# Optimization experiments

Hardware: AMD Instinct MI355X
Metric: run time of the kernel (lower is better)

The kernel has to match this reference:

```python
import jax, jax.numpy as jnp
import numpy as np

N = 100000


def gcn_conv(x, edge_index, W, b):
    """PyG GCNConv: h = D^-1/2 (A+I) D^-1/2 (x W) + b, scatter-add at targets."""
    n = x.shape[0]
    src, dst = edge_index[0], edge_index[1]
    # add self-loops
    loop = jnp.arange(n, dtype=src.dtype)
    src = jnp.concatenate([src, loop])
    dst = jnp.concatenate([dst, loop])
    # degree of target nodes (with self-loops), symmetric normalization
    deg = jax.ops.segment_sum(jnp.ones_like(dst, dtype=x.dtype), dst, num_segments=n)
    dinv = jnp.where(deg > 0, jax.lax.rsqrt(deg), 0.0)
    norm = dinv[src] * dinv[dst]                     # [E+N]
    h = x @ W                                        # [N, out] transform first (small dim)
    msg = h[src] * norm[:, None]                     # gather + scale
    out = jax.ops.segment_sum(msg, dst, num_segments=n)  # scatter-add
    return out + b


def setup_inputs() -> dict:
    key = jax.random.key(0)
    k1, k2, k3, k4, k5 = jax.random.split(key, 5)
    x = jax.random.normal(k1, (N, 128), dtype=jnp.float32)
    edge_index = jax.random.randint(k2, (2, 1600000), 0, N, dtype=jnp.int64)
    # glorot-ish init for linear weights, zero bias (PyG default)
    W1 = jax.random.normal(k3, (128, 64), dtype=jnp.float32) * (1.0 / np.sqrt(128))
    b1 = jnp.zeros((64,), dtype=jnp.float32)
    W2 = jax.random.normal(k4, (64, 32), dtype=jnp.float32) * (1.0 / np.sqrt(64))
    b2 = jnp.zeros((32,), dtype=jnp.float32)
    return {"x": x, "edge_index": edge_index, "W1": W1, "b1": b1, "W2": W2, "b2": b2}


def reference(x, edge_index, W1, b1, W2, b2):
    h = gcn_conv(x, edge_index, W1, b1)
    h = jax.nn.relu(h)
    # dropout is identity in eval mode (training=False)
    out = gcn_conv(h, edge_index, W2, b2)
    return out
```

## Files before the change

kernel.cpp:

```cpp
#include <hip/hip_runtime.h>

typedef unsigned int   u32;
typedef unsigned short u16;
typedef __attribute__((ext_vector_type(8))) short bf16x8;
typedef __attribute__((ext_vector_type(4))) float f32x4;

__device__ __forceinline__ u16 f2b(float f) {
    u32 u = __float_as_uint(f);
    u += 0x7FFFu + ((u >> 16) & 1u);
    return (u16)(u >> 16);
}
__device__ __forceinline__ float b2f_lo(u32 v) { return __uint_as_float(v << 16); }
__device__ __forceinline__ float b2f_hi(u32 v) { return __uint_as_float(v & 0xFFFF0000u); }
__device__ __forceinline__ u32 pack2(float a, float b) {
    return (u32)f2b(a) | ((u32)f2b(b) << 16);
}

#define BSHIFT 8
#define BIN_CHUNK 2048
#define CAP_MAX 6144


__global__ void k_init(const float* __restrict__ W1, bf16x8* __restrict__ Wpack,
                       int* __restrict__ bcnt, int NB) {
    int tid = threadIdx.x;
    for (int i = tid; i < NB; i += 256) bcnt[i] = 0;
    if (tid < 64) {
        int lane = tid;
#pragma unroll
        for (int ct = 0; ct < 4; ct++) {
#pragma unroll
            for (int ks = 0; ks < 4; ks++) {
                bf16x8 h;
#pragma unroll
                for (int j = 0; j < 8; j++) {
                    int k = ks * 32 + ((lane >> 4) << 3) + j;
                    int col = ct * 16 + (lane & 15);
                    h[j] = (short)f2b(W1[k * 64 + col]);
                }
                Wpack[(ct * 4 + ks) * 64 + lane] = h;
            }
        }
    }
}


__global__ __launch_bounds__(256) void k_bin(const int* __restrict__ src,
                                             const int* __restrict__ dst,
                                             int* __restrict__ bcnt,
                                             u32* __restrict__ binned,
                                             int E, int NB, int CAP) {
    __shared__ int lh[512], ls[512], gb[512], sh[256];
    __shared__ u32 stage[BIN_CHUNK];
    __shared__ u16 sbuck[BIN_CHUNK];
    int tid = threadIdx.x;
    int base = blockIdx.x * BIN_CHUNK;
    int cnt = E - base;
    if (cnt > BIN_CHUNK) cnt = BIN_CHUNK;

    for (int i = tid; i < 512; i += 256) lh[i] = 0;
    __syncthreads();

    const int T = BIN_CHUNK / 256;
    int bk[T], r[T];
    u32 key[T];
#pragma unroll
    for (int t = 0; t < T; t++) {
        int i = base + t * 256 + tid;
        bk[t] = -1;
        if (i < E) {
            int dv = dst[i];
            bk[t] = dv >> BSHIFT;
            key[t] = ((u32)(dv & 255) << 24) | (u32)src[i];
            r[t] = atomicAdd(&lh[bk[t]], 1);
        }
    }
    __syncthreads();
    {
        int a0 = lh[2 * tid], a1 = lh[2 * tid + 1];
        int sum2 = a0 + a1;
        sh[tid] = sum2;
        __syncthreads();
        for (int dd = 1; dd < 256; dd <<= 1) {
            int x = tid >= dd ? sh[tid - dd] : 0;
            __syncthreads();
            sh[tid] += x;
            __syncthreads();
        }
        int excl = sh[tid] - sum2;
        ls[2 * tid] = excl;
        ls[2 * tid + 1] = excl + a0;
    }
    for (int b = tid; b < NB; b += 256) {
        int c = lh[b];
        gb[b] = c ? atomicAdd(&bcnt[b], c) : 0;
    }
    __syncthreads();
#pragma unroll
    for (int t = 0; t < T; t++) {
        if (bk[t] >= 0) {
            int slot = ls[bk[t]] + r[t];
            stage[slot] = key[t];
            sbuck[slot] = (u16)bk[t];
        }
    }
    __syncthreads();
    for (int j = tid; j < cnt; j += 256) {
        u32 e = stage[j];
        int b = sbuck[j];
        int p = gb[b] + (j - ls[b]);
        if (p < CAP) binned[(size_t)b * CAP + p] = e;
    }
}


__global__ __launch_bounds__(256) void k_csr_gemm1(const u32* __restrict__ binned,
                                                   const int* __restrict__ bcnt,
                                                   const bf16x8* __restrict__ Wpack,
                                                   const float* __restrict__ x,
                                                   float* __restrict__ dinv,
                                                   int2* __restrict__ offse,
                                                   int* __restrict__ esrc,
                                                   u16* __restrict__ h1b,
                                                   int n, int CAP) {
    __shared__ u32 stagec[CAP_MAX];
    __shared__ int lcnt[256], lcur[256], sh[256];
    __shared__ float dinv_sh[256];
    int tid = threadIdx.x;
    int b = blockIdx.x;
    size_t base = (size_t)b * CAP;
    int nodeBase = b << BSHIFT;
    int ecnt = bcnt[b];
    if (ecnt > CAP) ecnt = CAP;
    lcnt[tid] = 0;
    __syncthreads();
    for (int j = tid; j < ecnt; j += 256) {
        u32 e = binned[base + j];
        stagec[j] = e;
        atomicAdd(&lcnt[e >> 24], 1);
    }
    __syncthreads();
    int v = lcnt[tid];
    sh[tid] = v;
    __syncthreads();
    for (int d = 1; d < 256; d <<= 1) {
        int xx = tid >= d ? sh[tid - d] : 0;
        __syncthreads();
        sh[tid] += xx;
        __syncthreads();
    }
    int excl = sh[tid] - v;
    int node = nodeBase + tid;
    float dvt = rsqrtf((float)(v + 1));
    dinv_sh[tid] = dvt;
    if (node < n) {
        offse[node] = make_int2((int)base + excl, (int)base + excl + v);
        dinv[node] = dvt;
    }
    lcur[tid] = excl;
    __syncthreads();
    for (int j = tid; j < ecnt; j += 256) {
        u32 e = stagec[j];
        int p = atomicAdd(&lcur[e >> 24], 1);
        esrc[base + p] = (int)(e & 0xFFFFFFu);
    }

    int wv = tid >> 6, lane = tid & 63;
    bf16x8 bfr[16];
#pragma unroll
    for (int f = 0; f < 16; f++) bfr[f] = Wpack[f * 64 + lane];

    for (int t = wv; t < 16; t += 4) {
        int rowBase = nodeBase + t * 16;
        if (rowBase >= n) break;
        f32x4 acc[4];
#pragma unroll
        for (int ct = 0; ct < 4; ct++) acc[ct] = (f32x4){0.f, 0.f, 0.f, 0.f};

        int r0 = rowBase + (lane & 15);
        if (r0 >= n) r0 = n - 1;
        const float* xr = x + (size_t)r0 * 128 + ((lane >> 4) << 3);
#pragma unroll
        for (int ks = 0; ks < 4; ks++) {
            float4 p0 = *(const float4*)(xr + ks * 32);
            float4 p1 = *(const float4*)(xr + ks * 32 + 4);
            bf16x8 a;
            a[0] = (short)f2b(p0.x); a[1] = (short)f2b(p0.y);
            a[2] = (short)f2b(p0.z); a[3] = (short)f2b(p0.w);
            a[4] = (short)f2b(p1.x); a[5] = (short)f2b(p1.y);
            a[6] = (short)f2b(p1.z); a[7] = (short)f2b(p1.w);
#pragma unroll
            for (int ct = 0; ct < 4; ct++)
                acc[ct] = __builtin_amdgcn_mfma_f32_16x16x32_bf16(a, bfr[ct * 4 + ks], acc[ct], 0, 0, 0);
        }
        int lrb = t * 16 + ((lane >> 4) << 2);
#pragma unroll
        for (int r = 0; r < 4; r++) {
            int lrow = lrb + r;
            int row = nodeBase + lrow;
            float dv = dinv_sh[lrow];
#pragma unroll
            for (int ct = 0; ct < 4; ct++) {
                float o = acc[ct][r] * dv;
                float onb = __shfl_xor(o, 1);
                if (!(lane & 1) && row < n) {
                    *(u32*)&h1b[(size_t)row * 64 + ct * 16 + (lane & 15)] = pack2(o, onb);
                }
            }
        }
    }
}


__global__ __launch_bounds__(256) void k_agg1gemm2(const u16* __restrict__ h1b,
                                                   const int2* __restrict__ offse,
                                                   const int* __restrict__ esrc,
                                                   const float* __restrict__ dinv,
                                                   const float* __restrict__ b1,
                                                   const float* __restrict__ W2,
                                                   u16* __restrict__ h2b, int n) {
    __shared__ float aggL[4][64];
    int warp = threadIdx.x >> 6, lane = threadIdx.x & 63;
    int half = lane >> 5, c2 = lane & 31;
    float w2r[32];
#pragma unroll
    for (int kk = 0; kk < 32; kk++) w2r[kk] = W2[(half * 32 + kk) * 32 + c2];
    float2 bb = *(const float2*)&b1[2 * c2];
    int nwaves = (gridDim.x * blockDim.x) >> 6;
    for (int wid = (int)((blockIdx.x * blockDim.x + threadIdx.x) >> 6); wid < n;
         wid += nwaves) {
        int2 ov = offse[wid];
        int e1 = ov.y;
        float a0 = 0.f, a1 = 0.f, a2 = 0.f, a3 = 0.f;
        if (half == 0) {
            u32 v = *(const u32*)&h1b[(size_t)wid * 64 + 2 * c2];
            a0 += b2f_lo(v); a1 += b2f_hi(v);
        }
        int e = ov.x + half;
        for (; e + 2 < e1; e += 4) {
            int s0 = esrc[e], s1 = esrc[e + 2];
            u32 v0 = *(const u32*)&h1b[(size_t)s0 * 64 + 2 * c2];
            u32 v1 = *(const u32*)&h1b[(size_t)s1 * 64 + 2 * c2];
            a0 += b2f_lo(v0); a1 += b2f_hi(v0);
            a2 += b2f_lo(v1); a3 += b2f_hi(v1);
        }
        if (e < e1) {
            int s = esrc[e];
            u32 v = *(const u32*)&h1b[(size_t)s * 64 + 2 * c2];
            a0 += b2f_lo(v); a1 += b2f_hi(v);
        }
        a0 += a2; a1 += a3;
        a0 += __shfl_xor(a0, 32);
        a1 += __shfl_xor(a1, 32);
        float dv = dinv[wid];
        a0 = a0 * dv + bb.x; a1 = a1 * dv + bb.y;
        a0 = a0 > 0.f ? a0 : 0.f;
        a1 = a1 > 0.f ? a1 : 0.f;
        if (half == 0) *(float2*)&aggL[warp][2 * c2] = make_float2(a0, a1);
        asm volatile("s_waitcnt lgkmcnt(0)" ::: "memory");
        float acc = 0.f;
#pragma unroll
        for (int kk = 0; kk < 32; kk += 4) {
            float4 av = *(const float4*)&aggL[warp][half * 32 + kk];
            acc += av.x * w2r[kk] + av.y * w2r[kk + 1] + av.z * w2r[kk + 2] + av.w * w2r[kk + 3];
        }
        acc += __shfl_xor(acc, 32);
        if (half == 0) h2b[(size_t)wid * 32 + c2] = f2b(acc * dv);
    }
}


__global__ __launch_bounds__(256) void k_agg2(const u16* __restrict__ h2b,
                                              const int2* __restrict__ offse,
                                              const int* __restrict__ esrc,
                                              const float* __restrict__ dinv,
                                              const float* __restrict__ b2,
                                              float* __restrict__ out, int n) {
    int wid = (int)((blockIdx.x * blockDim.x + threadIdx.x) >> 6);
    int lane = threadIdx.x & 63;
    int g = lane >> 4, c2 = lane & 15;
    if (wid >= n) return;
    int2 ov = offse[wid];
    int e1 = ov.y;
    float a0 = 0.f, a1 = 0.f, a2 = 0.f, a3 = 0.f;
    int e = ov.x + g;
    for (; e + 4 < e1; e += 8) {
        int s0 = esrc[e], s1 = esrc[e + 4];
        u32 v0 = *(const u32*)&h2b[(size_t)s0 * 32 + 2 * c2];
        u32 v1 = *(const u32*)&h2b[(size_t)s1 * 32 + 2 * c2];
        a0 += b2f_lo(v0); a1 += b2f_hi(v0);
        a2 += b2f_lo(v1); a3 += b2f_hi(v1);
    }
    if (e < e1) {
        int s = esrc[e];
        u32 v = *(const u32*)&h2b[(size_t)s * 32 + 2 * c2];
        a0 += b2f_lo(v); a1 += b2f_hi(v);
    }
    a0 += a2; a1 += a3;
    a0 += __shfl_xor(a0, 16); a0 += __shfl_xor(a0, 32);
    a1 += __shfl_xor(a1, 16); a1 += __shfl_xor(a1, 32);
    if (g == 0) {
        u32 v = *(const u32*)&h2b[(size_t)wid * 32 + 2 * c2];
        a0 += b2f_lo(v); a1 += b2f_hi(v);
        float dv = dinv[wid];
        float2 o = make_float2(a0 * dv + b2[2 * c2], a1 * dv + b2[2 * c2 + 1]);
        *(float2*)&out[(size_t)wid * 32 + 2 * c2] = o;
    }
}


extern "C" void kernel_launch(void* const* d_in, const int* in_sizes, int n_in,
                              void* d_out, int out_size, void* d_ws, size_t ws_size,
                              hipStream_t stream) {
    const float* x  = (const float*)d_in[0];
    const int*   ei = (const int*)d_in[1];
    const float* W1 = (const float*)d_in[2];
    const float* b1 = (const float*)d_in[3];
    const float* W2 = (const float*)d_in[4];
    const float* b2 = (const float*)d_in[5];
    float* out = (float*)d_out;

    const int n = in_sizes[0] / 128;
    const int E = in_sizes[1] / 2;
    const int* src = ei;
    const int* dst = ei + E;
    const int NB = (n + 255) >> BSHIFT;
    int avg = (E + NB - 1) / NB;
    int CAP = avg + avg / 8 + 512;
    if (CAP > CAP_MAX) CAP = CAP_MAX;

    char* ws = (char*)d_ws;
    size_t woff = 0;
    auto carve = [&](size_t bytes) {
        void* p = ws + woff;
        woff += (bytes + 255) & ~(size_t)255;
        return p;
    };
    int*    bcnt   = (int*)carve((size_t)NB * sizeof(int));
    u32*    binned = (u32*)carve((size_t)NB * CAP * sizeof(u32));
    int2*   offse  = (int2*)carve((size_t)n * sizeof(int2));
    float*  dinv   = (float*)carve((size_t)n * sizeof(float));
    int*    esrc   = (int*)carve((size_t)NB * CAP * sizeof(int));
    bf16x8* Wpack  = (bf16x8*)carve(16 * 64 * sizeof(bf16x8));
    u16*    h1b    = (u16*)carve((size_t)n * 64 * sizeof(u16));
    u16*    h2b    = (u16*)carve((size_t)n * 32 * sizeof(u16));

    const int B = 256;

    k_init<<<1, B, 0, stream>>>(W1, Wpack, bcnt, NB);

    k_bin<<<(E + BIN_CHUNK - 1) / BIN_CHUNK, B, 0, stream>>>(src, dst, bcnt, binned, E, NB, CAP);

    k_csr_gemm1<<<NB, B, 0, stream>>>(binned, bcnt, Wpack, x, dinv, offse, esrc, h1b, n, CAP);

    k_agg1gemm2<<<2048, B, 0, stream>>>(h1b, offse, esrc, dinv, b1, W2, h2b, n);

    k_agg2<<<(n + 3) / 4, B, 0, stream>>>(h2b, offse, esrc, dinv, b2, out, n);
}
```

Measured before the change: 164.7 us.

## Split layer-1 aggregation into column-chunked gathers and an MFMA GEMM2

```diff
diff --git a/kernel.cpp b/kernel.cpp
--- a/kernel.cpp
+++ b/kernel.cpp
@@ -21,7 +21,8 @@
 #define CAP_MAX 6144
 
 
-__global__ void k_init(const float* __restrict__ W1, bf16x8* __restrict__ Wpack,
+__global__ void k_init(const float* __restrict__ W1, const float* __restrict__ W2,
+                       bf16x8* __restrict__ Wpack, bf16x8* __restrict__ W2pack,
                        int* __restrict__ bcnt, int NB) {
     int tid = threadIdx.x;
     for (int i = tid; i < NB; i += 256) bcnt[i] = 0;
@@ -39,6 +40,20 @@
                     h[j] = (short)f2b(W1[k * 64 + col]);
                 }
                 Wpack[(ct * 4 + ks) * 64 + lane] = h;
+            }
+        }
+#pragma unroll
+        for (int ct = 0; ct < 2; ct++) {
+#pragma unroll
+            for (int ks = 0; ks < 2; ks++) {
+                bf16x8 h;
+#pragma unroll
+                for (int j = 0; j < 8; j++) {
+                    int k = ks * 32 + ((lane >> 4) << 3) + j;
+                    int col = ct * 16 + (lane & 15);
+                    h[j] = (short)f2b(W2[k * 32 + col]);
+                }
+                W2pack[(ct * 2 + ks) * 64 + lane] = h;
             }
         }
     }
@@ -169,6 +184,7 @@
     bf16x8 bfr[16];
 #pragma unroll
     for (int f = 0; f < 16; f++) bfr[f] = Wpack[f * 64 + lane];
+    size_t cs = (size_t)n * 16;
 
     for (int t = wv; t < 16; t += 4) {
         int rowBase = nodeBase + t * 16;
@@ -204,7 +220,7 @@
                 float o = acc[ct][r] * dv;
                 float onb = __shfl_xor(o, 1);
                 if (!(lane & 1) && row < n) {
-                    *(u32*)&h1b[(size_t)row * 64 + ct * 16 + (lane & 15)] = pack2(o, onb);
+                    *(u32*)&h1b[(size_t)ct * cs + (size_t)row * 16 + (lane & 15)] = pack2(o, onb);
                 }
             }
         }
@@ -212,60 +228,94 @@
 }
 
 
-__global__ __launch_bounds__(256) void k_agg1gemm2(const u16* __restrict__ h1b,
-                                                   const int2* __restrict__ offse,
-                                                   const int* __restrict__ esrc,
-                                                   const float* __restrict__ dinv,
-                                                   const float* __restrict__ b1,
-                                                   const float* __restrict__ W2,
-                                                   u16* __restrict__ h2b, int n) {
-    __shared__ float aggL[4][64];
-    int warp = threadIdx.x >> 6, lane = threadIdx.x & 63;
-    int half = lane >> 5, c2 = lane & 31;
-    float w2r[32];
-#pragma unroll
-    for (int kk = 0; kk < 32; kk++) w2r[kk] = W2[(half * 32 + kk) * 32 + c2];
-    float2 bb = *(const float2*)&b1[2 * c2];
-    int nwaves = (gridDim.x * blockDim.x) >> 6;
-    for (int wid = (int)((blockIdx.x * blockDim.x + threadIdx.x) >> 6); wid < n;
-         wid += nwaves) {
-        int2 ov = offse[wid];
-        int e1 = ov.y;
-        float a0 = 0.f, a1 = 0.f, a2 = 0.f, a3 = 0.f;
-        if (half == 0) {
-            u32 v = *(const u32*)&h1b[(size_t)wid * 64 + 2 * c2];
-            a0 += b2f_lo(v); a1 += b2f_hi(v);
-        }
-        int e = ov.x + half;
-        for (; e + 2 < e1; e += 4) {
-            int s0 = esrc[e], s1 = esrc[e + 2];
-            u32 v0 = *(const u32*)&h1b[(size_t)s0 * 64 + 2 * c2];
-            u32 v1 = *(const u32*)&h1b[(size_t)s1 * 64 + 2 * c2];
-            a0 += b2f_lo(v0); a1 += b2f_hi(v0);
-            a2 += b2f_lo(v1); a3 += b2f_hi(v1);
-        }
-        if (e < e1) {
-            int s = esrc[e];
-            u32 v = *(const u32*)&h1b[(size_t)s * 64 + 2 * c2];
-            a0 += b2f_lo(v); a1 += b2f_hi(v);
-        }
-        a0 += a2; a1 += a3;
-        a0 += __shfl_xor(a0, 32);
-        a1 += __shfl_xor(a1, 32);
-        float dv = dinv[wid];
-        a0 = a0 * dv + bb.x; a1 = a1 * dv + bb.y;
-        a0 = a0 > 0.f ? a0 : 0.f;
-        a1 = a1 > 0.f ? a1 : 0.f;
-        if (half == 0) *(float2*)&aggL[warp][2 * c2] = make_float2(a0, a1);
-        asm volatile("s_waitcnt lgkmcnt(0)" ::: "memory");
-        float acc = 0.f;
-#pragma unroll
-        for (int kk = 0; kk < 32; kk += 4) {
-            float4 av = *(const float4*)&aggL[warp][half * 32 + kk];
-            acc += av.x * w2r[kk] + av.y * w2r[kk + 1] + av.z * w2r[kk + 2] + av.w * w2r[kk + 3];
-        }
-        acc += __shfl_xor(acc, 32);
-        if (half == 0) h2b[(size_t)wid * 32 + c2] = f2b(acc * dv);
+__global__ __launch_bounds__(256) void k_gather1(const u16* __restrict__ h1c,
+                                                 const int2* __restrict__ offse,
+                                                 const int* __restrict__ esrc,
+                                                 float* __restrict__ aggc,
+                                                 int n) {
+    int node = (int)((blockIdx.x * blockDim.x + threadIdx.x) >> 5);
+    if (node >= n) return;
+    int l = threadIdx.x & 31;
+    int slot = l >> 3;
+    int j = l & 7;
+    int2 ov = offse[node];
+    float a0 = 0.f, a1 = 0.f;
+    for (int e = ov.x + slot; e < ov.y; e += 4) {
+        int s = esrc[e];
+        u32 v = *(const u32*)&h1c[(size_t)s * 16 + 2 * j];
+        a0 += b2f_lo(v); a1 += b2f_hi(v);
+    }
+    a0 += __shfl_xor(a0, 8);  a1 += __shfl_xor(a1, 8);
+    a0 += __shfl_xor(a0, 16); a1 += __shfl_xor(a1, 16);
+    if (slot == 0) {
+        u32 v = *(const u32*)&h1c[(size_t)node * 16 + 2 * j];
+        a0 += b2f_lo(v); a1 += b2f_hi(v);
+        *(float2*)&aggc[(size_t)node * 16 + 2 * j] = make_float2(a0, a1);
+    }
+}
+
+
+__global__ __launch_bounds__(256) void k_gemm2_mfma(const float* __restrict__ agg,
+                                                    const float* __restrict__ dinv,
+                                                    const float* __restrict__ b1,
+                                                    const bf16x8* __restrict__ W2pack,
+                                                    u16* __restrict__ h2b,
+                                                    int n, int ntiles) {
+    int gwave = (int)((blockIdx.x * blockDim.x + threadIdx.x) >> 6);
+    int lane = threadIdx.x & 63;
+    if (gwave >= ntiles) return;
+    int rowBase = gwave * 16;
+
+    bf16x8 bfr[4];
+#pragma unroll
+    for (int f = 0; f < 4; f++) bfr[f] = W2pack[f * 64 + lane];
+    float b1r[16];
+#pragma unroll
+    for (int ks = 0; ks < 2; ks++)
+#pragma unroll
+        for (int j = 0; j < 8; j++)
+            b1r[ks * 8 + j] = b1[ks * 32 + ((lane >> 4) << 3) + j];
+
+    int r0 = rowBase + (lane & 15);
+    if (r0 >= n) r0 = n - 1;
+    float dv0 = dinv[r0];
+    size_t cs = (size_t)n * 16;
+
+    f32x4 acc[2];
+    acc[0] = (f32x4){0.f, 0.f, 0.f, 0.f};
+    acc[1] = (f32x4){0.f, 0.f, 0.f, 0.f};
+#pragma unroll
+    for (int ks = 0; ks < 2; ks++) {
+        int c0 = 2 * ks + ((lane >> 4) >> 1);
+        int j0 = ((lane >> 4) & 1) << 3;
+        const float* ap = agg + (size_t)c0 * cs + (size_t)r0 * 16 + j0;
+        float4 p0 = *(const float4*)ap;
+        float4 p1 = *(const float4*)(ap + 4);
+        float t[8] = {p0.x, p0.y, p0.z, p0.w, p1.x, p1.y, p1.z, p1.w};
+        bf16x8 a;
+#pragma unroll
+        for (int j = 0; j < 8; j++) {
+            float av = t[j] * dv0 + b1r[ks * 8 + j];
+            a[j] = (short)f2b(av > 0.f ? av : 0.f);
+        }
+#pragma unroll
+        for (int ct = 0; ct < 2; ct++)
+            acc[ct] = __builtin_amdgcn_mfma_f32_16x16x32_bf16(a, bfr[ct * 2 + ks], acc[ct], 0, 0, 0);
+    }
+
+    int rbase = rowBase + ((lane >> 4) << 2);
+#pragma unroll
+    for (int r = 0; r < 4; r++) {
+        int row = rbase + r;
+        float dv = (row < n) ? dinv[row] : 0.f;
+#pragma unroll
+        for (int ct = 0; ct < 2; ct++) {
+            float o = acc[ct][r] * dv;
+            float onb = __shfl_xor(o, 1);
+            if (!(lane & 1) && row < n) {
+                *(u32*)&h2b[(size_t)row * 32 + ct * 16 + (lane & 15)] = pack2(o, onb);
+            }
+        }
     }
 }
 
@@ -342,18 +392,27 @@
     float*  dinv   = (float*)carve((size_t)n * sizeof(float));
     int*    esrc   = (int*)carve((size_t)NB * CAP * sizeof(int));
     bf16x8* Wpack  = (bf16x8*)carve(16 * 64 * sizeof(bf16x8));
+    bf16x8* W2pack = (bf16x8*)carve(4 * 64 * sizeof(bf16x8));
     u16*    h1b    = (u16*)carve((size_t)n * 64 * sizeof(u16));
+    float*  agg    = (float*)carve((size_t)n * 64 * sizeof(float));
     u16*    h2b    = (u16*)carve((size_t)n * 32 * sizeof(u16));
 
     const int B = 256;
 
-    k_init<<<1, B, 0, stream>>>(W1, Wpack, bcnt, NB);
+    k_init<<<1, B, 0, stream>>>(W1, W2, Wpack, W2pack, bcnt, NB);
 
     k_bin<<<(E + BIN_CHUNK - 1) / BIN_CHUNK, B, 0, stream>>>(src, dst, bcnt, binned, E, NB, CAP);
 
     k_csr_gemm1<<<NB, B, 0, stream>>>(binned, bcnt, Wpack, x, dinv, offse, esrc, h1b, n, CAP);
 
-    k_agg1gemm2<<<2048, B, 0, stream>>>(h1b, offse, esrc, dinv, b1, W2, h2b, n);
+    size_t cs = (size_t)n * 16;
+    int gGather = (n + 7) / 8;
+    for (int p = 0; p < 4; p++) {
+        k_gather1<<<gGather, B, 0, stream>>>(h1b + p * cs, offse, esrc, agg + p * cs, n);
+    }
+
+    int ntiles2 = (n + 15) / 16;
+    k_gemm2_mfma<<<(ntiles2 + 3) / 4, B, 0, stream>>>(agg, dinv, b1, W2pack, h2b, n, ntiles2);
 
     k_agg2<<<(n + 3) / 4, B, 0, stream>>>(h2b, offse, esrc, dinv, b2, out, n);
 }
```

New measurement: 225.9 us. 37.2% more time.

## Pad CSR edge lists to multiples of eight with zero sentinel row

Applied to the files above, without the earlier changes.

```diff
diff --git a/kernel.cpp b/kernel.cpp
--- a/kernel.cpp
+++ b/kernel.cpp
@@ -19,12 +19,16 @@
 #define BSHIFT 8
 #define BIN_CHUNK 2048
 #define CAP_MAX 6144
+#define PAD_EXTRA 2048
 
 
 __global__ void k_init(const float* __restrict__ W1, bf16x8* __restrict__ Wpack,
-                       int* __restrict__ bcnt, int NB) {
+                       int* __restrict__ bcnt, int NB,
+                       u16* __restrict__ h1b, u16* __restrict__ h2b, int n) {
     int tid = threadIdx.x;
     for (int i = tid; i < NB; i += 256) bcnt[i] = 0;
+    if (tid >= 64 && tid < 96)  ((u32*)&h1b[(size_t)n * 64])[tid - 64] = 0;
+    if (tid >= 96 && tid < 112) ((u32*)&h2b[(size_t)n * 32])[tid - 96] = 0;
     if (tid < 64) {
         int lane = tid;
 #pragma unroll
@@ -122,13 +126,14 @@
                                                    int2* __restrict__ offse,
                                                    int* __restrict__ esrc,
                                                    u16* __restrict__ h1b,
-                                                   int n, int CAP) {
+                                                   int n, int CAP, int CAPP) {
     __shared__ u32 stagec[CAP_MAX];
     __shared__ int lcnt[256], lcur[256], sh[256];
     __shared__ float dinv_sh[256];
     int tid = threadIdx.x;
     int b = blockIdx.x;
     size_t base = (size_t)b * CAP;
+    size_t basep = (size_t)b * CAPP;
     int nodeBase = b << BSHIFT;
     int ecnt = bcnt[b];
     if (ecnt > CAP) ecnt = CAP;
@@ -141,7 +146,8 @@
     }
     __syncthreads();
     int v = lcnt[tid];
-    sh[tid] = v;
+    int vp = (v + 7) & ~7;
+    sh[tid] = vp;
     __syncthreads();
     for (int d = 1; d < 256; d <<= 1) {
         int xx = tid >= d ? sh[tid - d] : 0;
@@ -149,12 +155,12 @@
         sh[tid] += xx;
         __syncthreads();
     }
-    int excl = sh[tid] - v;
+    int excl = sh[tid] - vp;
     int node = nodeBase + tid;
     float dvt = rsqrtf((float)(v + 1));
     dinv_sh[tid] = dvt;
     if (node < n) {
-        offse[node] = make_int2((int)base + excl, (int)base + excl + v);
+        offse[node] = make_int2((int)basep + excl, (int)basep + excl + v);
         dinv[node] = dvt;
     }
     lcur[tid] = excl;
@@ -162,8 +168,9 @@
     for (int j = tid; j < ecnt; j += 256) {
         u32 e = stagec[j];
         int p = atomicAdd(&lcur[e >> 24], 1);
-        esrc[base + p] = (int)(e & 0xFFFFFFu);
-    }
+        esrc[basep + p] = (int)(e & 0xFFFFFFu);
+    }
+    for (int j = excl + v; j < excl + vp; j++) esrc[basep + j] = n;
 
     int wv = tid >> 6, lane = tid & 63;
     bf16x8 bfr[16];
@@ -230,26 +237,27 @@
     for (int wid = (int)((blockIdx.x * blockDim.x + threadIdx.x) >> 6); wid < n;
          wid += nwaves) {
         int2 ov = offse[wid];
-        int e1 = ov.y;
+        int lenp = ((ov.y - ov.x) + 7) & ~7;
+        int eend = ov.x + lenp;
         float a0 = 0.f, a1 = 0.f, a2 = 0.f, a3 = 0.f;
+        float a4 = 0.f, a5 = 0.f, a6 = 0.f, a7 = 0.f;
         if (half == 0) {
             u32 v = *(const u32*)&h1b[(size_t)wid * 64 + 2 * c2];
             a0 += b2f_lo(v); a1 += b2f_hi(v);
         }
-        int e = ov.x + half;
-        for (; e + 2 < e1; e += 4) {
-            int s0 = esrc[e], s1 = esrc[e + 2];
+        for (int e = ov.x + half; e < eend; e += 8) {
+            int s0 = esrc[e], s1 = esrc[e + 2], s2 = esrc[e + 4], s3 = esrc[e + 6];
             u32 v0 = *(const u32*)&h1b[(size_t)s0 * 64 + 2 * c2];
             u32 v1 = *(const u32*)&h1b[(size_t)s1 * 64 + 2 * c2];
+            u32 v2 = *(const u32*)&h1b[(size_t)s2 * 64 + 2 * c2];
+            u32 v3 = *(const u32*)&h1b[(size_t)s3 * 64 + 2 * c2];
             a0 += b2f_lo(v0); a1 += b2f_hi(v0);
             a2 += b2f_lo(v1); a3 += b2f_hi(v1);
-        }
-        if (e < e1) {
-            int s = esrc[e];
-            u32 v = *(const u32*)&h1b[(size_t)s * 64 + 2 * c2];
-            a0 += b2f_lo(v); a1 += b2f_hi(v);
-        }
-        a0 += a2; a1 += a3;
+            a4 += b2f_lo(v2); a5 += b2f_hi(v2);
+            a6 += b2f_lo(v3); a7 += b2f_hi(v3);
+        }
+        a0 += a2 + a4 + a6;
+        a1 += a3 + a5 + a7;
         a0 += __shfl_xor(a0, 32);
         a1 += __shfl_xor(a1, 32);
         float dv = dinv[wid];
@@ -281,20 +289,15 @@
     int g = lane >> 4, c2 = lane & 15;
     if (wid >= n) return;
     int2 ov = offse[wid];
-    int e1 = ov.y;
+    int lenp = ((ov.y - ov.x) + 7) & ~7;
+    int eend = ov.x + lenp;
     float a0 = 0.f, a1 = 0.f, a2 = 0.f, a3 = 0.f;
-    int e = ov.x + g;
-    for (; e + 4 < e1; e += 8) {
+    for (int e = ov.x + g; e < eend; e += 8) {
         int s0 = esrc[e], s1 = esrc[e + 4];
         u32 v0 = *(const u32*)&h2b[(size_t)s0 * 32 + 2 * c2];
         u32 v1 = *(const u32*)&h2b[(size_t)s1 * 32 + 2 * c2];
         a0 += b2f_lo(v0); a1 += b2f_hi(v0);
         a2 += b2f_lo(v1); a3 += b2f_hi(v1);
-    }
-    if (e < e1) {
-        int s = esrc[e];
-        u32 v = *(const u32*)&h2b[(size_t)s * 32 + 2 * c2];
-        a0 += b2f_lo(v); a1 += b2f_hi(v);
     }
     a0 += a2; a1 += a3;
     a0 += __shfl_xor(a0, 16); a0 += __shfl_xor(a0, 32);
@@ -328,6 +331,7 @@
     int avg = (E + NB - 1) / NB;
     int CAP = avg + avg / 8 + 512;
     if (CAP > CAP_MAX) CAP = CAP_MAX;
+    int CAPP = CAP + PAD_EXTRA;
 
     char* ws = (char*)d_ws;
     size_t woff = 0;
@@ -340,18 +344,18 @@
     u32*    binned = (u32*)carve((size_t)NB * CAP * sizeof(u32));
     int2*   offse  = (int2*)carve((size_t)n * sizeof(int2));
     float*  dinv   = (float*)carve((size_t)n * sizeof(float));
-    int*    esrc   = (int*)carve((size_t)NB * CAP * sizeof(int));
+    int*    esrc   = (int*)carve((size_t)NB * CAPP * sizeof(int));
     bf16x8* Wpack  = (bf16x8*)carve(16 * 64 * sizeof(bf16x8));
-    u16*    h1b    = (u16*)carve((size_t)n * 64 * sizeof(u16));
-    u16*    h2b    = (u16*)carve((size_t)n * 32 * sizeof(u16));
+    u16*    h1b    = (u16*)carve((size_t)(n + 1) * 64 * sizeof(u16));
+    u16*    h2b    = (u16*)carve((size_t)(n + 1) * 32 * sizeof(u16));
 
     const int B = 256;
 
-    k_init<<<1, B, 0, stream>>>(W1, Wpack, bcnt, NB);
+    k_init<<<1, B, 0, stream>>>(W1, Wpack, bcnt, NB, h1b, h2b, n);
 
     k_bin<<<(E + BIN_CHUNK - 1) / BIN_CHUNK, B, 0, stream>>>(src, dst, bcnt, binned, E, NB, CAP);
 
-    k_csr_gemm1<<<NB, B, 0, stream>>>(binned, bcnt, Wpack, x, dinv, offse, esrc, h1b, n, CAP);
+    k_csr_gemm1<<<NB, B, 0, stream>>>(binned, bcnt, Wpack, x, dinv, offse, esrc, h1b, n, CAP, CAPP);
 
     k_agg1gemm2<<<2048, B, 0, stream>>>(h1b, offse, esrc, dinv, b1, W2, h2b, n);
 
```

Measured after the change: 169.3 us. +2.8%, slower.
